# Optimization experiments

Hardware: AMD Instinct MI355X
Metric: run time of the kernel (lower is better)

The kernel has to match this reference:

```python
import jax, jax.numpy as jnp
import numpy as np

N = 8192  # number of ReLU nodes; abstract matrices are (N+1)x(N+1)


def setup_inputs() -> dict:
    key = jax.random.key(0)
    k1, k2 = jax.random.split(key)
    a = jax.random.normal(k1, (N,), dtype=jnp.float32)
    b = jax.random.normal(k2, (N,), dtype=jnp.float32)
    lower = jnp.minimum(a, b)
    upper = jnp.maximum(a, b)
    # alphas initialized exactly as in the module: 1e-5 if u < -l else 1.0
    alphas = jnp.where(upper < -lower, jnp.float32(1e-5), jnp.float32(1.0))
    return {"lower": lower, "upper": upper, "alphas": alphas}


def reference(lower, upper, alphas):
    n = lower.shape[0]
    l, u = lower, upper
    active = (u > 0) & (l >= 0)      # identity relaxation
    unstable = (u > 0) & (l < 0)     # triangle relaxation; u <= 0 -> all zeros
    a = jnp.clip(alphas, 0.0, 1.0)
    denom = u - l
    lam = u / jnp.where(denom == 0, jnp.ones_like(denom), denom)

    diag_low = jnp.where(active, 1.0, jnp.where(unstable, a, 0.0))
    diag_up = jnp.where(active, 1.0, jnp.where(unstable, lam, 0.0))
    bias_up = jnp.where(unstable, -lam * l, 0.0)  # last-row bias of upper relaxation

    conc_low = jnp.where(active, l, jnp.where(unstable, a * l, 0.0))
    conc_up = jnp.where(u > 0, u, 0.0)

    idx = jnp.arange(n)
    A_low = (jnp.zeros((n + 1, n + 1), dtype=lower.dtype)
             .at[idx, idx].set(diag_low)
             .at[n, n].set(1.0))
    A_up = (jnp.zeros((n + 1, n + 1), dtype=lower.dtype)
            .at[idx, idx].set(diag_up)
            .at[n, :n].set(bias_up)
            .at[n, n].set(1.0))
    return conc_low, conc_up, A_low, A_up
```

## Files before the change

### kernel.cpp

```cpp
#include <hip/hip_runtime.h>


__global__ void relu_relax_kernel(const float* __restrict__ lower,
                                  const float* __restrict__ upper,
                                  const float* __restrict__ alphas,
                                  float* __restrict__ out,
                                  int n) {
    int i = blockIdx.x * blockDim.x + threadIdx.x;
    if (i >= n) return;

    const size_t np1 = (size_t)n + 1;
    const size_t AL = 2 * (size_t)n;
    const size_t AU = AL + np1 * np1;

    float l = lower[i];
    float u = upper[i];
    float a = alphas[i];
    a = fminf(fmaxf(a, 0.f), 1.f);

    bool active   = (u > 0.f) && (l >= 0.f);
    bool unstable = (u > 0.f) && (l < 0.f);

    float denom = u - l;
    float lam = u / ((denom == 0.f) ? 1.f : denom);

    float diag_low = active ? 1.f : (unstable ? a   : 0.f);
    float diag_up  = active ? 1.f : (unstable ? lam : 0.f);
    float bias_up  = unstable ? (-lam * l) : 0.f;
    float conc_low = active ? l : (unstable ? (a * l) : 0.f);
    float conc_up  = (u > 0.f) ? u : 0.f;

    out[i]              = conc_low;
    out[(size_t)n + i]  = conc_up;
    out[AL + (size_t)i * (np1 + 1)] = diag_low;
    out[AU + (size_t)i * (np1 + 1)] = diag_up;
    out[AU + (size_t)n * np1 + i]   = bias_up;

    if (i == 0) {
        out[AL + np1 * np1 - 1] = 1.f;
        out[AU + np1 * np1 - 1] = 1.f;
    }
}

extern "C" void kernel_launch(void* const* d_in, const int* in_sizes, int n_in,
                              void* d_out, int out_size, void* d_ws, size_t ws_size,
                              hipStream_t stream) {
    const float* lower  = (const float*)d_in[0];
    const float* upper  = (const float*)d_in[1];
    const float* alphas = (const float*)d_in[2];
    float* out = (float*)d_out;

    const int n = in_sizes[0];
    const size_t total = (size_t)out_size;

    hipMemsetAsync(out, 0, total * sizeof(float), stream);

    relu_relax_kernel<<<(n + 255) / 256, 256, 0, stream>>>(lower, upper, alphas, out, n);
}
```

Measured before the change: 518.1 us.

## Fuse zero-fill and diagonal writes into one vectorized nontemporal kernel

Replaces the separate hipMemsetAsync plus scatter kernel with a single grid-stride kernel that writes every output element once. It uses float4 nontemporal stores and computes the diagonal, bias-row and concatenated entries inline, with a specialization templated on the matrix size. This removes the second pass over the diagonal and the extra launch. The cost is per-vector index division and a slow path for chunks touching the diagonal or the last row, which is extra work next to a plain memset.

New measurement: 556.7 us. 1.07x slower.

```diff
diff --git a/kernel.cpp b/kernel.cpp
--- a/kernel.cpp
+++ b/kernel.cpp
@@ -1,44 +1,138 @@
 #include <hip/hip_runtime.h>
+#include <stdint.h>
 
 
-__global__ void relu_relax_kernel(const float* __restrict__ lower,
-                                  const float* __restrict__ upper,
-                                  const float* __restrict__ alphas,
-                                  float* __restrict__ out,
-                                  int n) {
-    int i = blockIdx.x * blockDim.x + threadIdx.x;
-    if (i >= n) return;
+typedef float f32x4 __attribute__((ext_vector_type(4)));
 
-    const size_t np1 = (size_t)n + 1;
-    const size_t AL = 2 * (size_t)n;
-    const size_t AU = AL + np1 * np1;
+struct NodeVals { float diag_low, diag_up, bias_up, conc_low, conc_up; };
 
-    float l = lower[i];
-    float u = upper[i];
-    float a = alphas[i];
-    a = fminf(fmaxf(a, 0.f), 1.f);
-
+__device__ __forceinline__ NodeVals node_vals(float l, float u, float a_raw) {
+    NodeVals nv;
+    float a = fminf(fmaxf(a_raw, 0.f), 1.f);
     bool active   = (u > 0.f) && (l >= 0.f);
     bool unstable = (u > 0.f) && (l < 0.f);
-
     float denom = u - l;
     float lam = u / ((denom == 0.f) ? 1.f : denom);
+    nv.diag_low = active ? 1.f : (unstable ? a : 0.f);
+    nv.diag_up  = active ? 1.f : (unstable ? lam : 0.f);
+    nv.bias_up  = unstable ? (-lam * l) : 0.f;
+    nv.conc_low = active ? l : (unstable ? (a * l) : 0.f);
+    nv.conc_up  = (u > 0.f) ? u : 0.f;
+    return nv;
+}
 
-    float diag_low = active ? 1.f : (unstable ? a   : 0.f);
-    float diag_up  = active ? 1.f : (unstable ? lam : 0.f);
-    float bias_up  = unstable ? (-lam * l) : 0.f;
-    float conc_low = active ? l : (unstable ? (a * l) : 0.f);
-    float conc_up  = (u > 0.f) ? u : 0.f;
+template <uint32_t NP1>
+__global__ __launch_bounds__(256) void fused_fill(
+        const float* __restrict__ lower,
+        const float* __restrict__ upper,
+        const float* __restrict__ alphas,
+        float* __restrict__ out) {
+    constexpr uint32_t N    = NP1 - 1;
+    constexpr size_t   NPSQ = (size_t)NP1 * NP1;
+    constexpr size_t   CONC = 2 * (size_t)N;
+    constexpr size_t   T    = CONC + 2 * NPSQ;
+    constexpr size_t   C4   = T / 4;
+    static_assert(CONC % 4 == 0, "conc region must be float4-aligned");
+    static_assert(T % 4 == 2, "tail handling assumes 2 trailing elements");
 
-    out[i]              = conc_low;
-    out[(size_t)n + i]  = conc_up;
-    out[AL + (size_t)i * (np1 + 1)] = diag_low;
-    out[AU + (size_t)i * (np1 + 1)] = diag_up;
-    out[AU + (size_t)n * np1 + i]   = bias_up;
+    f32x4* __restrict__ out4 = (f32x4*)out;
+    const size_t stride = (size_t)gridDim.x * blockDim.x;
 
-    if (i == 0) {
-        out[AL + np1 * np1 - 1] = 1.f;
-        out[AU + np1 * np1 - 1] = 1.f;
+    for (size_t j = (size_t)blockIdx.x * blockDim.x + threadIdx.x; j < C4; j += stride) {
+        const size_t e0 = j * 4;
+        f32x4 v = (f32x4){0.f, 0.f, 0.f, 0.f};
+
+        if (e0 < CONC) {
+            if (e0 < (size_t)N) {
+                const f32x4 l4 = *(const f32x4*)(lower  + e0);
+                const f32x4 u4 = *(const f32x4*)(upper  + e0);
+                const f32x4 a4 = *(const f32x4*)(alphas + e0);
+                v[0] = node_vals(l4[0], u4[0], a4[0]).conc_low;
+                v[1] = node_vals(l4[1], u4[1], a4[1]).conc_low;
+                v[2] = node_vals(l4[2], u4[2], a4[2]).conc_low;
+                v[3] = node_vals(l4[3], u4[3], a4[3]).conc_low;
+            } else {
+                const f32x4 u4 = *(const f32x4*)(upper + (e0 - N));
+                v[0] = (u4[0] > 0.f) ? u4[0] : 0.f;
+                v[1] = (u4[1] > 0.f) ? u4[1] : 0.f;
+                v[2] = (u4[2] > 0.f) ? u4[2] : 0.f;
+                v[3] = (u4[3] > 0.f) ? u4[3] : 0.f;
+            }
+        } else {
+            const size_t g = e0 - CONC;
+            int      mat = (g >= NPSQ) ? 1 : 0;
+            uint32_t h   = (uint32_t)(mat ? (g - NPSQ) : g);
+            uint32_t r   = h / NP1;
+            uint32_t c   = h - r * NP1;
+
+            const bool slow = (c > (uint32_t)(NP1 - 4)) |
+                              ((uint32_t)(r - c) <= 3u) |
+                              ((mat != 0) & (r == N));
+            if (slow) {
+                int m_ = mat; uint32_t rr = r, cc = c;
+                #pragma unroll
+                for (int k = 0; k < 4; ++k) {
+                    float val = 0.f;
+                    if (rr == cc) {
+                        if (rr == N) {
+                            val = 1.f;
+                        } else {
+                            NodeVals nv = node_vals(lower[rr], upper[rr], alphas[rr]);
+                            val = m_ ? nv.diag_up : nv.diag_low;
+                        }
+                    } else if (m_ && rr == N) {
+                        NodeVals nv = node_vals(lower[cc], upper[cc], alphas[cc]);
+                        val = nv.bias_up;
+                    }
+                    v[k] = val;
+                    ++cc;
+                    if (cc == NP1) { cc = 0; ++rr; if (rr == NP1) { rr = 0; m_ = 1; } }
+                }
+            }
+        }
+        __builtin_nontemporal_store(v, out4 + j);
+    }
+
+    if (blockIdx.x == 0 && threadIdx.x == 0) {
+        NodeVals nv = node_vals(lower[N - 1], upper[N - 1], alphas[N - 1]);
+        out[T - 2] = nv.bias_up;
+        out[T - 1] = 1.f;
+    }
+}
+
+__global__ void generic_fill(const float* __restrict__ lower,
+                             const float* __restrict__ upper,
+                             const float* __restrict__ alphas,
+                             float* __restrict__ out, int n) {
+    const uint32_t np1  = (uint32_t)n + 1;
+    const size_t   npsq = (size_t)np1 * np1;
+    const size_t   conc = 2 * (size_t)n;
+    const size_t   T    = conc + 2 * npsq;
+    const size_t stride = (size_t)gridDim.x * blockDim.x;
+    for (size_t e = (size_t)blockIdx.x * blockDim.x + threadIdx.x; e < T; e += stride) {
+        float val = 0.f;
+        if (e < (size_t)n) {
+            val = node_vals(lower[e], upper[e], alphas[e]).conc_low;
+        } else if (e < conc) {
+            size_t i = e - n;
+            val = node_vals(lower[i], upper[i], alphas[i]).conc_up;
+        } else {
+            size_t g = e - conc;
+            int mat = (g >= npsq) ? 1 : 0;
+            size_t h = mat ? (g - npsq) : g;
+            uint32_t r = (uint32_t)(h / np1);
+            uint32_t c = (uint32_t)(h - (size_t)r * np1);
+            if (r == c) {
+                if (r == (uint32_t)n) val = 1.f;
+                else {
+                    NodeVals nv = node_vals(lower[r], upper[r], alphas[r]);
+                    val = mat ? nv.diag_up : nv.diag_low;
+                }
+            } else if (mat && r == (uint32_t)n) {
+                val = node_vals(lower[c], upper[c], alphas[c]).bias_up;
+            }
+        }
+        out[e] = val;
     }
 }
 
@@ -49,11 +143,11 @@
     const float* upper  = (const float*)d_in[1];
     const float* alphas = (const float*)d_in[2];
     float* out = (float*)d_out;
+    const int n = in_sizes[0];
 
-    const int n = in_sizes[0];
-    const size_t total = (size_t)out_size;
-
-    hipMemsetAsync(out, 0, total * sizeof(float), stream);
-
-    relu_relax_kernel<<<(n + 255) / 256, 256, 0, stream>>>(lower, upper, alphas, out, n);
+    if (n == 8192) {
+        fused_fill<8193><<<4096, 256, 0, stream>>>(lower, upper, alphas, out);
+    } else {
+        generic_fill<<<2048, 256, 0, stream>>>(lower, upper, alphas, out, n);
+    }
 }
```
